# Performance work log

Hardware: AMD Instinct MI355X
Metric: run time of the kernel (lower is better)

Reference implementation:

```python
import jax, jax.numpy as jnp
import numpy as np

E = 1024        # embedding_dim
DIN = 2048      # d_inner = E * expand_factor(2)
N = 16          # state_dim
DTR = 64        # dt_rank = ceil(E/16)
K_CONV = 4      # conv_dim


def tt_dense(g1, g2):
    # TT with ranks [1,16,1]: W[(m1,m2),(n1,n2)] = sum_r g1[m1,n1,r] g2[r,m2,n2]
    m1, n1, r = g1.shape
    _, m2, n2 = g2.shape
    return jnp.einsum('air,rbj->abij', g1, g2).reshape(m1 * m2, n1 * n2)


def setup_inputs() -> dict:
    key = jax.random.key(0)
    ks = jax.random.split(key, 12)
    s = 0.05  # init scale for TT cores
    return {
        'x': jax.random.normal(ks[0], (2, 1024, E), dtype=jnp.float32),
        # in_proj: 1024=[32,32] -> 4096=[64,64]
        'in_g1': jax.random.normal(ks[1], (32, 64, 16)) * s,
        'in_g2': jax.random.normal(ks[2], (16, 32, 64)) * s,
        # x_proj: 2048=[32,64] -> 96=[8,12]
        'x_g1': jax.random.normal(ks[3], (32, 8, 16)) * s,
        'x_g2': jax.random.normal(ks[4], (16, 64, 12)) * s,
        # dt_proj: 64=[8,8] -> 2048=[32,64]
        'dt_g1': jax.random.normal(ks[5], (8, 32, 16)) * s,
        'dt_g2': jax.random.normal(ks[6], (16, 8, 64)) * s,
        # out_proj: 2048=[32,64] -> 1024=[32,32]
        'out_g1': jax.random.normal(ks[7], (32, 32, 16)) * s,
        'out_g2': jax.random.normal(ks[8], (16, 64, 32)) * s,
        'conv_filter': jax.random.normal(ks[9], (K_CONV, 1, DIN)) * 0.1,
        'conv_bias': jnp.zeros((DIN,), jnp.float32),
        'A_log': jax.random.uniform(ks[10], (DIN, N), dtype=jnp.float32),
        'D': jnp.zeros((DIN,), jnp.float32),
    }


def _forward(x, in_g1, in_g2, x_g1, x_g2, dt_g1, dt_g2, out_g1, out_g2,
             conv_filter, conv_bias, A_log, D):
    B, L, _ = x.shape
    # in_proj (TT) -> split into conv path and gate
    xz = (x.reshape(-1, E) @ tt_dense(in_g1, in_g2)).reshape(B, L, 2 * DIN)
    x_conv, z = xz[..., :DIN], xz[..., DIN:]
    # depthwise conv1d, SAME padding, + bias, SiLU, gate by z
    conv = jax.lax.conv_general_dilated(
        x_conv, conv_filter, window_strides=(1,), padding='SAME',
        dimension_numbers=('NWC', 'WIO', 'NWC'), feature_group_count=DIN)
    y = jax.nn.silu(conv + conv_bias) * z            # [B, L, DIN]
    # x_proj (TT) -> dt_unscaled, B, C
    dtBC = (y.reshape(-1, DIN) @ tt_dense(x_g1, x_g2)).reshape(B, L, DTR + 2 * N)
    dt_un = dtBC[..., :DTR]
    Bm = dtBC[..., DTR:DTR + N]                      # [B, L, N]
    Cm = dtBC[..., DTR + N:]                         # [B, L, N]
    # dt_proj (TT) + softplus
    dt = jax.nn.softplus(dt_un.reshape(-1, DTR) @ tt_dense(dt_g1, dt_g2)).reshape(B, L, DIN)
    # selective scan
    A = -jnp.exp(A_log)                              # [DIN, N]

    def step(h, inp):
        dt_t, u_t, B_t, C_t = inp                    # [B,DIN],[B,DIN],[B,N],[B,N]
        dA = jnp.exp(dt_t[:, :, None] * A)           # [B, DIN, N]
        h = dA * h + dt_t[:, :, None] * B_t[:, None, :] * u_t[:, :, None]
        y_t = jnp.einsum('bdn,bn->bd', h, C_t) + D * u_t
        return h, (y_t, h)

    h0 = jnp.zeros((B, DIN, N), x.dtype)
    _, (ys, hs) = jax.lax.scan(
        step, h0,
        (dt.swapaxes(0, 1), y.swapaxes(0, 1), Bm.swapaxes(0, 1), Cm.swapaxes(0, 1)))
    ssm_out = ys.swapaxes(0, 1) + jnp.mean(hs) * 1e-8  # [B, L, DIN]
    out = (ssm_out.reshape(-1, DIN) @ tt_dense(out_g1, out_g2)).reshape(B, L, E)
    return out


def reference(x, in_g1, in_g2, x_g1, x_g2, dt_g1, dt_g2, out_g1, out_g2,
              conv_filter, conv_bias, A_log, D):
    return _forward(x, in_g1, in_g2, x_g1, x_g2, dt_g1, dt_g2, out_g1, out_g2,
                    conv_filter, conv_bias, A_log, D)
```

## Files before the change

kernel.cpp:

```cpp
#include <hip/hip_runtime.h>
#include <hip/hip_bf16.h>
#include <cstdint>
#include <cstddef>

#define EE    1024
#define DIN   2048
#define NST   16
#define DTR   64
#define BB_   2
#define LL    1024
#define BL    (BB_*LL)
#define NCHUNK 32
#define CLEN   32
#define RTT   16

typedef unsigned short u16;
typedef unsigned int   u32;

static constexpr size_t OFF_WINT  = 0;
static constexpr size_t OFF_WOUTT = 2097152;
static constexpr size_t OFF_WXT   = 3145728;
static constexpr size_t OFF_WDTT  = 3276800;
static constexpr size_t OFF_A2T   = 3342336;
static constexpr size_t OFF_XB    = 3375104;
static constexpr size_t OFF_XZB   = 4423680;
static constexpr size_t OFF_YB    = 8617984;
static constexpr size_t OFF_PART  = 10715136;
static constexpr size_t OFF_DTBC  = 14909440;
static constexpr size_t OFF_DTUNB = 15106048;
static constexpr size_t OFF_DTB   = 15171584;
static constexpr size_t OFF_YSB   = 17268736;
static constexpr size_t OFF_HC    = 19365888;
static constexpr size_t OFF_SDT   = 21463040;

__device__ __forceinline__ u16 f2bf(float f) {
    u32 u = __float_as_uint(f);
    u += 0x7fffu + ((u >> 16) & 1u);
    return (u16)(u >> 16);
}
__device__ __forceinline__ float bf2f(u16 v) {
    return __uint_as_float((u32)v << 16);
}

__device__ __forceinline__ void async_copy16(const void* g, void* l) {
    __builtin_amdgcn_global_load_lds((const __attribute__((address_space(1))) u32*)g,
                                     (__attribute__((address_space(3))) u32*)l,
                                     16, 0, 0);
}

__device__ __forceinline__ float softplusf(float v) {
    return fmaxf(v, 0.f) + log1pf(__expf(-fabsf(v)));
}

__device__ void tt_part(const float* __restrict__ g1, const float* __restrict__ g2,
                        u16* __restrict__ Wt, int m1, int n1, int m2, int n2,
                        int c, int crows, float* g1col, float* g2col)
{
    const int rowsW = m1 * m2;
    if (c >= crows) {
        for (int k = threadIdx.x; k < rowsW; k += 256)
            Wt[(size_t)c * rowsW + k] = 0;
        return;
    }
    const int i = c / n2;
    const int j = c - i * n2;

    for (int e = threadIdx.x; e < m1 * RTT; e += 256) {
        const int a = e >> 4, rr = e & 15;
        g1col[e] = g1[(size_t)(a * n1 + i) * RTT + rr];
    }
    for (int e = threadIdx.x; e < RTT * m2; e += 256) {
        const int rr = e / m2, bb = e - rr * m2;
        g2col[e] = g2[(size_t)(rr * m2 + bb) * n2 + j];
    }
    __syncthreads();

    for (int k = threadIdx.x; k < rowsW; k += 256) {
        const int a  = k / m2;
        const int bb = k - a * m2;
        const float* gp = g1col + a * RTT;
        float s = 0.f;
        #pragma unroll
        for (int rr = 0; rr < RTT; ++rr)
            s = fmaf(gp[rr], g2col[rr * m2 + bb], s);
        Wt[(size_t)c * rowsW + k] = f2bf(s);
    }
}

__global__ __launch_bounds__(256) void mega_prep(
    const float* __restrict__ in_g1, const float* __restrict__ in_g2, u16* __restrict__ W_inT,
    const float* __restrict__ out_g1, const float* __restrict__ out_g2, u16* __restrict__ W_outT,
    const float* __restrict__ x_g1, const float* __restrict__ x_g2, u16* __restrict__ W_xT,
    const float* __restrict__ dt_g1, const float* __restrict__ dt_g2, u16* __restrict__ W_dtT,
    const float* __restrict__ x, u16* __restrict__ xb,
    const float* __restrict__ A_log, float* __restrict__ A2t)
{
    __shared__ float g1col[32 * RTT];
    __shared__ float g2col[RTT * 64];
    const int blk = blockIdx.x;
    if (blk < 4096) {
        tt_part(in_g1, in_g2, W_inT, 32, 64, 32, 64, blk, 4096, g1col, g2col);
    } else if (blk < 5120) {
        tt_part(out_g1, out_g2, W_outT, 32, 32, 64, 32, blk - 4096, 1024, g1col, g2col);
    } else if (blk < 5248) {
        tt_part(x_g1, x_g2, W_xT, 32, 8, 64, 12, blk - 5120, 96, g1col, g2col);
    } else if (blk < 7296) {
        tt_part(dt_g1, dt_g2, W_dtT, 8, 32, 8, 64, blk - 5248, 2048, g1col, g2col);
    } else if (blk < 9344) {
        const int i = (blk - 7296) * 256 + threadIdx.x;
        float4 v = ((const float4*)x)[i];
        ushort4 o;
        o.x = f2bf(v.x); o.y = f2bf(v.y); o.z = f2bf(v.z); o.w = f2bf(v.w);
        ((ushort4*)xb)[i] = o;
    } else {
        const int idx = (blk - 9344) * 256 + threadIdx.x;
        const int d = idx >> 4, n = idx & 15;
        A2t[n * DIN + d] = -expf(A_log[idx]);
    }
}

typedef __attribute__((ext_vector_type(8))) short bf16x8;
typedef __attribute__((ext_vector_type(4))) float floatx4;

template<int BN, int BK, int OUT>
__global__ __launch_bounds__(256) void gemm_bf16(
    const u16* __restrict__ A, const u16* __restrict__ Bt, void* __restrict__ Cout,
    int K, int ldc, int kchunk, size_t czstride)
{
    constexpr int BM   = 128;
    constexpr int NT   = BN / 32;
    constexpr int SLOT = BK / 8;
    constexpr int CR   = 64 / SLOT;
    constexpr int NACH = BM / CR / 4;
    constexpr int NBCH = BN / CR / 4;
    constexpr int KG   = BK / 32;
    __shared__ u16 As[BM * BK];
    __shared__ u16 Bs[BN * BK];

    const int tid  = threadIdx.x;
    const int w    = tid >> 6;
    const int lane = tid & 63;
    const int wm   = w & 1, wn = w >> 1;
    const int row0 = blockIdx.y * BM;
    const int col0 = blockIdx.x * BN;
    const int kbeg = blockIdx.z * kchunk;

    const int srow = lane / SLOT;
    const int kqp  = lane % SLOT;
    const u16* ga[NACH]; u16* la[NACH];
    #pragma unroll
    for (int i = 0; i < NACH; ++i) {
        const int c  = w * NACH + i;
        const int r  = c * CR + srow;
        const int kq = kqp ^ ((r >> 1) & (SLOT - 1));
        ga[i] = A + (size_t)(row0 + r) * K + kbeg + kq * 8;
        la[i] = &As[c * CR * BK];
    }
    const u16* gb[NBCH]; u16* lb[NBCH];
    #pragma unroll
    for (int i = 0; i < NBCH; ++i) {
        const int c  = w * NBCH + i;
        const int r  = c * CR + srow;
        const int kq = kqp ^ ((r >> 1) & (SLOT - 1));
        gb[i] = Bt + (size_t)(col0 + r) * K + kbeg + kq * 8;
        lb[i] = &Bs[c * CR * BK];
    }

    const int q = lane >> 4, l15 = lane & 15;
    int a_off[4][KG], b_off[NT][KG];
    #pragma unroll
    for (int mt = 0; mt < 4; ++mt) {
        const int r = wm * 64 + mt * 16 + l15;
        const int m = (r >> 1) & (SLOT - 1);
        #pragma unroll
        for (int kk = 0; kk < KG; ++kk)
            a_off[mt][kk] = r * BK + ((kk * 4 + q) ^ m) * 8;
    }
    #pragma unroll
    for (int nt = 0; nt < NT; ++nt) {
        const int r = wn * (BN / 2) + nt * 16 + l15;
        const int m = (r >> 1) & (SLOT - 1);
        #pragma unroll
        for (int kk = 0; kk < KG; ++kk)
            b_off[nt][kk] = r * BK + ((kk * 4 + q) ^ m) * 8;
    }

    floatx4 acc[4][NT];
    #pragma unroll
    for (int mt = 0; mt < 4; ++mt)
        #pragma unroll
        for (int nt = 0; nt < NT; ++nt)
            acc[mt][nt] = (floatx4){0.f, 0.f, 0.f, 0.f};

    for (int k0 = 0; k0 < kchunk; k0 += BK) {
        #pragma unroll
        for (int i = 0; i < NACH; ++i) { async_copy16(ga[i], la[i]); ga[i] += BK; }
        #pragma unroll
        for (int i = 0; i < NBCH; ++i) { async_copy16(gb[i], lb[i]); gb[i] += BK; }
        __syncthreads();

        bf16x8 af[4][KG], bfv[NT][KG];
        #pragma unroll
        for (int mt = 0; mt < 4; ++mt)
            #pragma unroll
            for (int kk = 0; kk < KG; ++kk)
                af[mt][kk] = *(const bf16x8*)&As[a_off[mt][kk]];
        #pragma unroll
        for (int nt = 0; nt < NT; ++nt)
            #pragma unroll
            for (int kk = 0; kk < KG; ++kk)
                bfv[nt][kk] = *(const bf16x8*)&Bs[b_off[nt][kk]];

        #pragma unroll
        for (int kk = 0; kk < KG; ++kk)
            #pragma unroll
            for (int mt = 0; mt < 4; ++mt)
                #pragma unroll
                for (int nt = 0; nt < NT; ++nt)
                    acc[mt][nt] = __builtin_amdgcn_mfma_f32_16x16x32_bf16(
                        af[mt][kk], bfv[nt][kk], acc[mt][nt], 0, 0, 0);

        __syncthreads();
    }

    #pragma unroll
    for (int mt = 0; mt < 4; ++mt) {
        const int row = row0 + wm * 64 + mt * 16 + q * 4;
        #pragma unroll
        for (int nt = 0; nt < NT; ++nt) {
            const int col = col0 + wn * (BN / 2) + nt * 16 + l15;
            #pragma unroll
            for (int r = 0; r < 4; ++r) {
                const float v = acc[mt][nt][r];
                if constexpr (OUT == 0) {
                    ((float*)Cout)[(size_t)blockIdx.z * czstride + (size_t)(row + r) * ldc + col] = v;
                } else if constexpr (OUT == 1) {
                    ((u16*)Cout)[(size_t)(row + r) * ldc + col] = f2bf(v);
                } else {
                    ((u16*)Cout)[(size_t)(row + r) * ldc + col] = f2bf(softplusf(v));
                }
            }
        }
    }
}

__global__ __launch_bounds__(256) void reduce_dtbc(
    const float* __restrict__ part, float* __restrict__ dtBC, u16* __restrict__ dtun_b)
{
    int idx = blockIdx.x * 256 + threadIdx.x;
    if (idx >= BL * 96) return;
    const int row = idx / 96;
    const int col = idx - row * 96;
    float s = 0.f;
    #pragma unroll
    for (int z = 0; z < 16; ++z)
        s += part[(size_t)z * BL * 128 + (size_t)row * 128 + col];
    dtBC[idx] = s;
    if (col < 64) dtun_b[(size_t)row * 64 + col] = f2bf(s);
}

__global__ __launch_bounds__(256) void reduce_out(
    const float* __restrict__ part, float* __restrict__ out)
{
    const int idx = blockIdx.x * 256 + threadIdx.x;
    const float4 a = ((const float4*)part)[idx];
    const float4 b = ((const float4*)part)[idx + BL * EE / 4];
    float4 o;
    o.x = a.x + b.x; o.y = a.y + b.y; o.z = a.z + b.z; o.w = a.w + b.w;
    ((float4*)out)[idx] = o;
}

typedef __attribute__((ext_vector_type(8))) unsigned short ushortx8;

__global__ __launch_bounds__(256) void conv_gate(
    const u16* __restrict__ xzb, const float* __restrict__ filt,
    const float* __restrict__ bias, u16* __restrict__ yb)
{
    int idx = blockIdx.x * blockDim.x + threadIdx.x;
    if (idx >= BL * DIN / 8) return;
    const int d  = (idx % (DIN / 8)) * 8;
    const int bt = idx / (DIN / 8);
    const int b  = bt >> 10;
    const int t  = bt & 1023;

    float acc[8];
    #pragma unroll
    for (int j = 0; j < 8; ++j) acc[j] = bias[d + j];
    #pragma unroll
    for (int k = 0; k < 4; ++k) {
        const int tt = t + k - 1;
        if ((unsigned)tt < (unsigned)LL) {
            const ushortx8 xc = *(const ushortx8*)(xzb + (size_t)(b * LL + tt) * (2 * DIN) + d);
            #pragma unroll
            for (int j = 0; j < 8; ++j)
                acc[j] = fmaf(bf2f(xc[j]), filt[(size_t)k * DIN + d + j], acc[j]);
        }
    }
    const ushortx8 z = *(const ushortx8*)(xzb + (size_t)bt * (2 * DIN) + DIN + d);
    ushortx8 o;
    #pragma unroll
    for (int j = 0; j < 8; ++j)
        o[j] = f2bf(acc[j] / (1.f + __expf(-acc[j])) * bf2f(z[j]));
    *(ushortx8*)(yb + (size_t)bt * DIN + d) = o;
}

__global__ __launch_bounds__(256) void scan_phase_a(
    const u16* __restrict__ dt, const u16* __restrict__ u,
    const float* __restrict__ dtBC, const float* __restrict__ A2t,
    float* __restrict__ hend, float* __restrict__ sdtbuf)
{
    const int d = blockIdx.x * 256 + threadIdx.x;
    const int c = blockIdx.y;
    const int b = blockIdx.z;

    __shared__ float Bs[CLEN][NST];
    for (int e = threadIdx.x; e < CLEN * NST; e += 256) {
        const int tl = e >> 4, n = e & 15;
        Bs[tl][n] = dtBC[(size_t)(b * LL + c * CLEN + tl) * 96 + 64 + n];
    }
    __syncthreads();

    float A2r[NST];
    #pragma unroll
    for (int n = 0; n < NST; ++n) A2r[n] = A2t[n * DIN + d];

    float h[NST] = {};
    float sdt = 0.f;
    const size_t tbase = (size_t)(b * LL + c * CLEN) * DIN + d;
    for (int tl = 0; tl < CLEN; ++tl) {
        const float dtv = bf2f(dt[tbase + (size_t)tl * DIN]);
        const float uv  = bf2f(u [tbase + (size_t)tl * DIN]);
        sdt += dtv;
        const float cu = dtv * uv;
        #pragma unroll
        for (int n = 0; n < NST; ++n) {
            const float a = __expf(A2r[n] * dtv);
            h[n] = fmaf(a, h[n], cu * Bs[tl][n]);
        }
    }
    const int cb = b * NCHUNK + c;
    #pragma unroll
    for (int n = 0; n < NST; ++n)
        hend[((size_t)cb * NST + n) * DIN + d] = h[n];
    sdtbuf[(size_t)cb * DIN + d] = sdt;
}

__global__ __launch_bounds__(256) void scan_phase_b(
    const float* __restrict__ A2t, const float* __restrict__ sdtbuf,
    float* __restrict__ hcarry)
{
    const int idx = blockIdx.x * 256 + threadIdx.x;
    if (idx >= BB_ * NST * DIN) return;
    const int d = idx & (DIN - 1);
    const int n = (idx >> 11) & 15;
    const int b = idx >> 15;
    const float A2 = A2t[n * DIN + d];
    float h = 0.f;
    for (int c = 0; c < NCHUNK; ++c) {
        const int cb = b * NCHUNK + c;
        const size_t off = ((size_t)cb * NST + n) * DIN + d;
        const float he = hcarry[off];
        const float pa = __expf(A2 * sdtbuf[(size_t)cb * DIN + d]);
        hcarry[off] = h;
        h = fmaf(pa, h, he);
    }
}

__global__ __launch_bounds__(256) void scan_phase_c(
    const u16* __restrict__ dt, const u16* __restrict__ u,
    const float* __restrict__ dtBC, const float* __restrict__ A2t,
    const float* __restrict__ hinit, const float* __restrict__ Dp,
    u16* __restrict__ ysb)
{
    const int d = blockIdx.x * 256 + threadIdx.x;
    const int c = blockIdx.y;
    const int b = blockIdx.z;

    __shared__ float Bs[CLEN][NST];
    __shared__ float Cs[CLEN][NST];
    for (int e = threadIdx.x; e < CLEN * NST; e += 256) {
        const int tl = e >> 4, n = e & 15;
        const size_t base = (size_t)(b * LL + c * CLEN + tl) * 96;
        Bs[tl][n] = dtBC[base + 64 + n];
        Cs[tl][n] = dtBC[base + 80 + n];
    }
    __syncthreads();

    float A2r[NST], h[NST];
    const int cb = b * NCHUNK + c;
    #pragma unroll
    for (int n = 0; n < NST; ++n) {
        A2r[n] = A2t[n * DIN + d];
        h[n]   = hinit[((size_t)cb * NST + n) * DIN + d];
    }
    const float Dv = Dp[d];

    const size_t tbase = (size_t)(b * LL + c * CLEN) * DIN + d;
    for (int tl = 0; tl < CLEN; ++tl) {
        const float dtv = bf2f(dt[tbase + (size_t)tl * DIN]);
        const float uv  = bf2f(u [tbase + (size_t)tl * DIN]);
        const float cu = dtv * uv;
        float yacc = 0.f;
        #pragma unroll
        for (int n = 0; n < NST; ++n) {
            const float a = __expf(A2r[n] * dtv);
            h[n] = fmaf(a, h[n], cu * Bs[tl][n]);
            yacc = fmaf(h[n], Cs[tl][n], yacc);
        }
        ysb[tbase + (size_t)tl * DIN] = f2bf(fmaf(Dv, uv, yacc));
    }
}

extern "C" void kernel_launch(void* const* d_in, const int* in_sizes, int n_in,
                              void* d_out, int out_size, void* d_ws, size_t ws_size,
                              hipStream_t stream)
{
    const float* x       = (const float*)d_in[0];
    const float* in_g1   = (const float*)d_in[1];
    const float* in_g2   = (const float*)d_in[2];
    const float* x_g1    = (const float*)d_in[3];
    const float* x_g2    = (const float*)d_in[4];
    const float* dt_g1   = (const float*)d_in[5];
    const float* dt_g2   = (const float*)d_in[6];
    const float* out_g1  = (const float*)d_in[7];
    const float* out_g2  = (const float*)d_in[8];
    const float* filt    = (const float*)d_in[9];
    const float* bias    = (const float*)d_in[10];
    const float* A_log   = (const float*)d_in[11];
    const float* Dp      = (const float*)d_in[12];

    float* ws     = (float*)d_ws;
    u16*   W_inT  = (u16*)(ws + OFF_WINT);
    u16*   W_outT = (u16*)(ws + OFF_WOUTT);
    u16*   W_xT   = (u16*)(ws + OFF_WXT);
    u16*   W_dtT  = (u16*)(ws + OFF_WDTT);
    float* A2t    = ws + OFF_A2T;
    u16*   xb     = (u16*)(ws + OFF_XB);
    u16*   xzb    = (u16*)(ws + OFF_XZB);
    u16*   yb     = (u16*)(ws + OFF_YB);
    float* part   = ws + OFF_PART;
    float* dtBC   = ws + OFF_DTBC;
    u16*   dtun_b = (u16*)(ws + OFF_DTUNB);
    u16*   dtb    = (u16*)(ws + OFF_DTB);
    u16*   ysb    = (u16*)(ws + OFF_YSB);
    float* hc     = ws + OFF_HC;
    float* sdt    = ws + OFF_SDT;

    mega_prep<<<9472, 256, 0, stream>>>(
        in_g1, in_g2, W_inT, out_g1, out_g2, W_outT,
        x_g1, x_g2, W_xT, dt_g1, dt_g2, W_dtT,
        x, xb, A_log, A2t);

    gemm_bf16<128, 64, 1><<<dim3(32, 16, 1), 256, 0, stream>>>(
        xb, W_inT, xzb, EE, 4096, EE, 0);

    conv_gate<<<(BL * DIN / 8 + 255) / 256, 256, 0, stream>>>(xzb, filt, bias, yb);

    gemm_bf16<128, 64, 0><<<dim3(1, 16, 16), 256, 0, stream>>>(
        yb, W_xT, part, DIN, 128, 128, (size_t)BL * 128);
    reduce_dtbc<<<(BL * 96 + 255) / 256, 256, 0, stream>>>(part, dtBC, dtun_b);

    gemm_bf16<128, 64, 2><<<dim3(16, 16, 1), 256, 0, stream>>>(
        dtun_b, W_dtT, dtb, 64, DIN, 64, 0);

    scan_phase_a<<<dim3(DIN / 256, NCHUNK, BB_), 256, 0, stream>>>(dtb, yb, dtBC, A2t, hc, sdt);
    scan_phase_b<<<(BB_ * NST * DIN) / 256, 256, 0, stream>>>(A2t, sdt, hc);
    scan_phase_c<<<dim3(DIN / 256, NCHUNK, BB_), 256, 0, stream>>>(dtb, yb, dtBC, A2t, hc, Dp, ysb);

    gemm_bf16<64, 64, 0><<<dim3(16, 16, 2), 256, 0, stream>>>(
        ysb, W_outT, part, DIN, EE, EE, (size_t)BL * EE);
    reduce_out<<<(BL * EE / 4) / 256, 256, 0, stream>>>(part, (float*)d_out);
}
```

Before: 228.3 us.

## Fuse dtBC reduce, dt_proj GEMM and three-phase scan into one cooperative kernel

Replaces five separate launches (reduce_dtbc, dt_proj GEMM, scan phases a/b/c) with a single cooperative kernel of 256 blocks that uses grid.sync between stages. Chunk length doubles to 64 with 16 chunks, and the dt values for each chunk are cached in shared memory so phase c reuses them instead of reloading. The aim is to remove launch gaps and inter-kernel drain. In exchange it runs far fewer blocks (256, about one per CU), which limits latency hiding in the scan, and it adds grid-wide barrier costs. It falls back to the old kernels if the cooperative launch fails.

```diff
diff --git a/kernel.cpp b/kernel.cpp
--- a/kernel.cpp
+++ b/kernel.cpp
@@ -1,7 +1,10 @@
 #include <hip/hip_runtime.h>
 #include <hip/hip_bf16.h>
+#include <hip/hip_cooperative_groups.h>
 #include <cstdint>
 #include <cstddef>
+
+namespace cg = cooperative_groups;
 
 #define EE    1024
 #define DIN   2048
@@ -12,6 +15,8 @@
 #define BL    (BB_*LL)
 #define NCHUNK 32
 #define CLEN   32
+#define NCHUNK_C 16
+#define CLEN_C   64
 #define RTT   16
 
 typedef unsigned short u16;
@@ -411,6 +416,196 @@
     }
 }
 
+struct CoopShm {
+    union {
+        struct { u16 As[128 * 64]; u16 Bs[128 * 64]; } g;
+        struct { float Bsc[CLEN_C][NST]; float Csc[CLEN_C][NST];
+                 u16 dtc[CLEN_C * 256]; } s;
+    };
+};
+
+__global__ __launch_bounds__(256) void coop_mid(
+    const float* __restrict__ part, float* __restrict__ dtBC, u16* __restrict__ dtun_b,
+    const u16* __restrict__ W_dtT, u16* __restrict__ dtb,
+    const u16* __restrict__ yb, const float* __restrict__ A2t,
+    float* __restrict__ hc, float* __restrict__ sdtg,
+    const float* __restrict__ Dp, u16* __restrict__ ysb)
+{
+    __shared__ CoopShm shm;
+    cg::grid_group grid = cg::this_grid();
+    const int blk = blockIdx.x;
+    const int tid = threadIdx.x;
+
+    #pragma unroll
+    for (int e = 0; e < 3; ++e) {
+        const int idx = blk * 768 + e * 256 + tid;
+        const int row = idx / 96;
+        const int col = idx - row * 96;
+        float s = 0.f;
+        #pragma unroll
+        for (int z = 0; z < 16; ++z)
+            s += part[(size_t)z * BL * 128 + (size_t)row * 128 + col];
+        dtBC[idx] = s;
+        if (col < 64) dtun_b[(size_t)row * 64 + col] = f2bf(s);
+    }
+    __threadfence();
+    grid.sync();
+
+    {
+        constexpr int BK = 64, SLOT = 8, CR = 8;
+        const int row0 = (blk >> 4) * 128;
+        const int col0 = (blk & 15) * 128;
+        const int w    = tid >> 6;
+        const int lane = tid & 63;
+        const int wm   = w & 1, wn = w >> 1;
+        const int srow = lane / SLOT;
+        const int kqp  = lane % SLOT;
+
+        #pragma unroll
+        for (int i = 0; i < 4; ++i) {
+            const int c  = w * 4 + i;
+            const int r  = c * CR + srow;
+            const int kq = kqp ^ ((r >> 1) & (SLOT - 1));
+            async_copy16(dtun_b + (size_t)(row0 + r) * 64 + kq * 8, &shm.g.As[c * CR * BK]);
+        }
+        #pragma unroll
+        for (int i = 0; i < 4; ++i) {
+            const int c  = w * 4 + i;
+            const int r  = c * CR + srow;
+            const int kq = kqp ^ ((r >> 1) & (SLOT - 1));
+            async_copy16(W_dtT + (size_t)(col0 + r) * 64 + kq * 8, &shm.g.Bs[c * CR * BK]);
+        }
+        __syncthreads();
+
+        const int q = lane >> 4, l15 = lane & 15;
+        floatx4 acc[4][4];
+        #pragma unroll
+        for (int mt = 0; mt < 4; ++mt)
+            #pragma unroll
+            for (int nt = 0; nt < 4; ++nt)
+                acc[mt][nt] = (floatx4){0.f, 0.f, 0.f, 0.f};
+
+        #pragma unroll
+        for (int kk = 0; kk < 2; ++kk) {
+            bf16x8 af[4], bfv[4];
+            #pragma unroll
+            for (int mt = 0; mt < 4; ++mt) {
+                const int r = wm * 64 + mt * 16 + l15;
+                af[mt] = *(const bf16x8*)&shm.g.As[r * BK + (((kk * 4 + q) ^ ((r >> 1) & 7)) * 8)];
+            }
+            #pragma unroll
+            for (int nt = 0; nt < 4; ++nt) {
+                const int r = wn * 64 + nt * 16 + l15;
+                bfv[nt] = *(const bf16x8*)&shm.g.Bs[r * BK + (((kk * 4 + q) ^ ((r >> 1) & 7)) * 8)];
+            }
+            #pragma unroll
+            for (int mt = 0; mt < 4; ++mt)
+                #pragma unroll
+                for (int nt = 0; nt < 4; ++nt)
+                    acc[mt][nt] = __builtin_amdgcn_mfma_f32_16x16x32_bf16(
+                        af[mt], bfv[nt], acc[mt][nt], 0, 0, 0);
+        }
+
+        #pragma unroll
+        for (int mt = 0; mt < 4; ++mt) {
+            const int row = row0 + wm * 64 + mt * 16 + q * 4;
+            #pragma unroll
+            for (int nt = 0; nt < 4; ++nt) {
+                const int col = col0 + wn * 64 + nt * 16 + l15;
+                #pragma unroll
+                for (int r = 0; r < 4; ++r)
+                    dtb[(size_t)(row + r) * DIN + col] = f2bf(softplusf(acc[mt][nt][r]));
+            }
+        }
+    }
+    __threadfence();
+    grid.sync();
+
+    const int db = blk & 7;
+    const int c  = (blk >> 3) & 15;
+    const int b  = blk >> 7;
+    const int d  = db * 256 + tid;
+    const int cb = b * NCHUNK_C + c;
+    const size_t tbase = (size_t)(b * LL + c * CLEN_C) * DIN + d;
+
+    float A2r[NST];
+    #pragma unroll
+    for (int n = 0; n < NST; ++n) A2r[n] = A2t[n * DIN + d];
+
+    {
+        for (int e = tid; e < CLEN_C * NST; e += 256) {
+            const int tl = e >> 4, n = e & 15;
+            const size_t base = (size_t)(b * LL + c * CLEN_C + tl) * 96;
+            shm.s.Bsc[tl][n] = dtBC[base + 64 + n];
+            shm.s.Csc[tl][n] = dtBC[base + 80 + n];
+        }
+        for (int tl = 0; tl < CLEN_C; ++tl)
+            shm.s.dtc[tl * 256 + tid] = dtb[tbase + (size_t)tl * DIN];
+        __syncthreads();
+
+        float h[NST] = {};
+        float sdt = 0.f;
+        for (int tl = 0; tl < CLEN_C; ++tl) {
+            const float dtv = bf2f(shm.s.dtc[tl * 256 + tid]);
+            const float uv  = bf2f(yb[tbase + (size_t)tl * DIN]);
+            sdt += dtv;
+            const float cu = dtv * uv;
+            #pragma unroll
+            for (int n = 0; n < NST; ++n) {
+                const float a = __expf(A2r[n] * dtv);
+                h[n] = fmaf(a, h[n], cu * shm.s.Bsc[tl][n]);
+            }
+        }
+        #pragma unroll
+        for (int n = 0; n < NST; ++n)
+            hc[((size_t)cb * NST + n) * DIN + d] = h[n];
+        sdtg[(size_t)cb * DIN + d] = sdt;
+    }
+    __threadfence();
+    grid.sync();
+
+    {
+        const int idx = blk * 256 + tid;
+        const int dd = idx & (DIN - 1);
+        const int nn = (idx >> 11) & 15;
+        const int bb = idx >> 15;
+        const float A2 = A2t[nn * DIN + dd];
+        float h = 0.f;
+        for (int cc = 0; cc < NCHUNK_C; ++cc) {
+            const int cbb = bb * NCHUNK_C + cc;
+            const size_t off = ((size_t)cbb * NST + nn) * DIN + dd;
+            const float he = hc[off];
+            const float pa = __expf(A2 * sdtg[(size_t)cbb * DIN + dd]);
+            hc[off] = h;
+            h = fmaf(pa, h, he);
+        }
+    }
+    __threadfence();
+    grid.sync();
+
+    {
+        float h[NST];
+        #pragma unroll
+        for (int n = 0; n < NST; ++n)
+            h[n] = hc[((size_t)cb * NST + n) * DIN + d];
+        const float Dv = Dp[d];
+
+        for (int tl = 0; tl < CLEN_C; ++tl) {
+            const float dtv = bf2f(shm.s.dtc[tl * 256 + tid]);
+            const float uv  = bf2f(yb[tbase + (size_t)tl * DIN]);
+            const float cu = dtv * uv;
+            float yacc = 0.f;
+            #pragma unroll
+            for (int n = 0; n < NST; ++n) {
+                const float a = __expf(A2r[n] * dtv);
+                h[n] = fmaf(a, h[n], cu * shm.s.Bsc[tl][n]);
+                yacc = fmaf(h[n], shm.s.Csc[tl][n], yacc);
+            }
+            ysb[tbase + (size_t)tl * DIN] = f2bf(fmaf(Dv, uv, yacc));
+        }
+    }
+}
+
 extern "C" void kernel_launch(void* const* d_in, const int* in_sizes, int n_in,
                               void* d_out, int out_size, void* d_ws, size_t ws_size,
                               hipStream_t stream)
@@ -444,7 +639,7 @@
     u16*   dtb    = (u16*)(ws + OFF_DTB);
     u16*   ysb    = (u16*)(ws + OFF_YSB);
     float* hc     = ws + OFF_HC;
-    float* sdt    = ws + OFF_SDT;
+    float* sdtg   = ws + OFF_SDT;
 
     mega_prep<<<9472, 256, 0, stream>>>(
         in_g1, in_g2, W_inT, out_g1, out_g2, W_outT,
@@ -458,14 +653,24 @@
 
     gemm_bf16<128, 64, 0><<<dim3(1, 16, 16), 256, 0, stream>>>(
         yb, W_xT, part, DIN, 128, 128, (size_t)BL * 128);
-    reduce_dtbc<<<(BL * 96 + 255) / 256, 256, 0, stream>>>(part, dtBC, dtun_b);
-
-    gemm_bf16<128, 64, 2><<<dim3(16, 16, 1), 256, 0, stream>>>(
-        dtun_b, W_dtT, dtb, 64, DIN, 64, 0);
-
-    scan_phase_a<<<dim3(DIN / 256, NCHUNK, BB_), 256, 0, stream>>>(dtb, yb, dtBC, A2t, hc, sdt);
-    scan_phase_b<<<(BB_ * NST * DIN) / 256, 256, 0, stream>>>(A2t, sdt, hc);
-    scan_phase_c<<<dim3(DIN / 256, NCHUNK, BB_), 256, 0, stream>>>(dtb, yb, dtBC, A2t, hc, Dp, ysb);
+
+    {
+        const float* part_c = part;
+        void* args[] = { (void*)&part_c, (void*)&dtBC, (void*)&dtun_b,
+                         (void*)&W_dtT, (void*)&dtb, (void*)&yb, (void*)&A2t,
+                         (void*)&hc, (void*)&sdtg, (void*)&Dp, (void*)&ysb };
+        hipError_t ce = hipLaunchCooperativeKernel((const void*)coop_mid, dim3(256),
+                                                   dim3(256), args, 0, stream);
+        if (ce != hipSuccess) {
+            (void)hipGetLastError();
+            reduce_dtbc<<<(BL * 96 + 255) / 256, 256, 0, stream>>>(part, dtBC, dtun_b);
+            gemm_bf16<128, 64, 2><<<dim3(16, 16, 1), 256, 0, stream>>>(
+                dtun_b, W_dtT, dtb, 64, DIN, 64, 0);
+            scan_phase_a<<<dim3(DIN / 256, NCHUNK, BB_), 256, 0, stream>>>(dtb, yb, dtBC, A2t, hc, sdtg);
+            scan_phase_b<<<(BB_ * NST * DIN) / 256, 256, 0, stream>>>(A2t, sdtg, hc);
+            scan_phase_c<<<dim3(DIN / 256, NCHUNK, BB_), 256, 0, stream>>>(dtb, yb, dtBC, A2t, hc, Dp, ysb);
+        }
+    }
 
     gemm_bf16<64, 64, 0><<<dim3(16, 16, 2), 256, 0, stream>>>(
         ysb, W_outT, part, DIN, EE, EE, (size_t)BL * EE);
```

New measurement: 455.2 us. 1.99x slower.

## Fuse chunk-carry scan into output scan phase by recomputing prefix per block

Applied to the files above, without the earlier changes.

Removes the separate sequential carry-propagation kernel. Each block of the output-scan phase now recomputes its own incoming state by iterating over all previous chunks' end states and summed dt. This drops one kernel launch and its serial 32-step latency, but adds redundant work that grows with chunk index: up to 31 chunks × 16 states of loads and exps per thread. Later chunks therefore do more carry work, so load across blocks becomes uneven.

```diff
diff --git a/kernel.cpp b/kernel.cpp
--- a/kernel.cpp
+++ b/kernel.cpp
@@ -345,32 +345,11 @@
     sdtbuf[(size_t)cb * DIN + d] = sdt;
 }
 
-__global__ __launch_bounds__(256) void scan_phase_b(
-    const float* __restrict__ A2t, const float* __restrict__ sdtbuf,
-    float* __restrict__ hcarry)
-{
-    const int idx = blockIdx.x * 256 + threadIdx.x;
-    if (idx >= BB_ * NST * DIN) return;
-    const int d = idx & (DIN - 1);
-    const int n = (idx >> 11) & 15;
-    const int b = idx >> 15;
-    const float A2 = A2t[n * DIN + d];
-    float h = 0.f;
-    for (int c = 0; c < NCHUNK; ++c) {
-        const int cb = b * NCHUNK + c;
-        const size_t off = ((size_t)cb * NST + n) * DIN + d;
-        const float he = hcarry[off];
-        const float pa = __expf(A2 * sdtbuf[(size_t)cb * DIN + d]);
-        hcarry[off] = h;
-        h = fmaf(pa, h, he);
-    }
-}
-
-__global__ __launch_bounds__(256) void scan_phase_c(
+__global__ __launch_bounds__(256) void scan_phase_bc(
     const u16* __restrict__ dt, const u16* __restrict__ u,
     const float* __restrict__ dtBC, const float* __restrict__ A2t,
-    const float* __restrict__ hinit, const float* __restrict__ Dp,
-    u16* __restrict__ ysb)
+    const float* __restrict__ hend, const float* __restrict__ sdtbuf,
+    const float* __restrict__ Dp, u16* __restrict__ ysb)
 {
     const int d = blockIdx.x * 256 + threadIdx.x;
     const int c = blockIdx.y;
@@ -386,12 +365,19 @@
     }
     __syncthreads();
 
-    float A2r[NST], h[NST];
-    const int cb = b * NCHUNK + c;
-    #pragma unroll
-    for (int n = 0; n < NST; ++n) {
-        A2r[n] = A2t[n * DIN + d];
-        h[n]   = hinit[((size_t)cb * NST + n) * DIN + d];
+    float A2r[NST];
+    #pragma unroll
+    for (int n = 0; n < NST; ++n) A2r[n] = A2t[n * DIN + d];
+
+    float h[NST] = {};
+    for (int cc = 0; cc < c; ++cc) {
+        const int cbb = b * NCHUNK + cc;
+        const float sdtv = sdtbuf[(size_t)cbb * DIN + d];
+        #pragma unroll
+        for (int n = 0; n < NST; ++n) {
+            const float pa = __expf(A2r[n] * sdtv);
+            h[n] = fmaf(pa, h[n], hend[((size_t)cbb * NST + n) * DIN + d]);
+        }
     }
     const float Dv = Dp[d];
 
@@ -444,7 +430,7 @@
     u16*   dtb    = (u16*)(ws + OFF_DTB);
     u16*   ysb    = (u16*)(ws + OFF_YSB);
     float* hc     = ws + OFF_HC;
-    float* sdt    = ws + OFF_SDT;
+    float* sdtg   = ws + OFF_SDT;
 
     mega_prep<<<9472, 256, 0, stream>>>(
         in_g1, in_g2, W_inT, out_g1, out_g2, W_outT,
@@ -463,9 +449,8 @@
     gemm_bf16<128, 64, 2><<<dim3(16, 16, 1), 256, 0, stream>>>(
         dtun_b, W_dtT, dtb, 64, DIN, 64, 0);
 
-    scan_phase_a<<<dim3(DIN / 256, NCHUNK, BB_), 256, 0, stream>>>(dtb, yb, dtBC, A2t, hc, sdt);
-    scan_phase_b<<<(BB_ * NST * DIN) / 256, 256, 0, stream>>>(A2t, sdt, hc);
-    scan_phase_c<<<dim3(DIN / 256, NCHUNK, BB_), 256, 0, stream>>>(dtb, yb, dtBC, A2t, hc, Dp, ysb);
+    scan_phase_a<<<dim3(DIN / 256, NCHUNK, BB_), 256, 0, stream>>>(dtb, yb, dtBC, A2t, hc, sdtg);
+    scan_phase_bc<<<dim3(DIN / 256, NCHUNK, BB_), 256, 0, stream>>>(dtb, yb, dtBC, A2t, hc, sdtg, Dp, ysb);
 
     gemm_bf16<64, 64, 0><<<dim3(16, 16, 2), 256, 0, stream>>>(
         ysb, W_outT, part, DIN, EE, EE, (size_t)BL * EE);
```

Result: slower. 240.8 us (+5.5%).

## Halve scan chunk length and process two channels per thread

Applied to the files above, without the earlier changes.

The chunked selective scan now uses 64 chunks of 16 steps instead of 32 of 32, so the serial per-thread dependency chain in the two per-chunk scan passes is shorter. Each thread now handles two adjacent channels, using packed 32-bit bf16 loads and stores and float2 stores for the carried state. This keeps the grid size constant while raising per-thread independent work. The trade-off is more register pressure, a longer sequential loop over chunks in the carry-propagation pass, and a larger carry buffer, which pushes the sdt workspace offset further out.

```diff
diff --git a/kernel.cpp b/kernel.cpp
--- a/kernel.cpp
+++ b/kernel.cpp
@@ -10,8 +10,8 @@
 #define BB_   2
 #define LL    1024
 #define BL    (BB_*LL)
-#define NCHUNK 32
-#define CLEN   32
+#define NCHUNK 64
+#define CLEN   16
 #define RTT   16
 
 typedef unsigned short u16;
@@ -31,7 +31,7 @@
 static constexpr size_t OFF_DTB   = 15171584;
 static constexpr size_t OFF_YSB   = 17268736;
 static constexpr size_t OFF_HC    = 19365888;
-static constexpr size_t OFF_SDT   = 21463040;
+static constexpr size_t OFF_SDT   = 23560192;
 
 __device__ __forceinline__ u16 f2bf(float f) {
     u32 u = __float_as_uint(f);
@@ -309,40 +309,47 @@
     const float* __restrict__ dtBC, const float* __restrict__ A2t,
     float* __restrict__ hend, float* __restrict__ sdtbuf)
 {
-    const int d = blockIdx.x * 256 + threadIdx.x;
+    const int d0 = blockIdx.x * 512 + threadIdx.x * 2;
     const int c = blockIdx.y;
     const int b = blockIdx.z;
 
     __shared__ float Bs[CLEN][NST];
-    for (int e = threadIdx.x; e < CLEN * NST; e += 256) {
+    {
+        const int e = threadIdx.x;
         const int tl = e >> 4, n = e & 15;
         Bs[tl][n] = dtBC[(size_t)(b * LL + c * CLEN + tl) * 96 + 64 + n];
     }
     __syncthreads();
 
-    float A2r[NST];
-    #pragma unroll
-    for (int n = 0; n < NST; ++n) A2r[n] = A2t[n * DIN + d];
-
-    float h[NST] = {};
-    float sdt = 0.f;
-    const size_t tbase = (size_t)(b * LL + c * CLEN) * DIN + d;
+    float A2r0[NST], A2r1[NST];
+    #pragma unroll
+    for (int n = 0; n < NST; ++n) {
+        A2r0[n] = A2t[n * DIN + d0];
+        A2r1[n] = A2t[n * DIN + d0 + 1];
+    }
+
+    float h0[NST] = {}, h1[NST] = {};
+    float sdt0 = 0.f, sdt1 = 0.f;
+    const size_t tbase = (size_t)(b * LL + c * CLEN) * DIN + d0;
+    #pragma unroll
     for (int tl = 0; tl < CLEN; ++tl) {
-        const float dtv = bf2f(dt[tbase + (size_t)tl * DIN]);
-        const float uv  = bf2f(u [tbase + (size_t)tl * DIN]);
-        sdt += dtv;
-        const float cu = dtv * uv;
+        const u32 dp = *(const u32*)(dt + tbase + (size_t)tl * DIN);
+        const u32 up = *(const u32*)(u  + tbase + (size_t)tl * DIN);
+        const float dtv0 = bf2f((u16)dp), dtv1 = bf2f((u16)(dp >> 16));
+        const float uv0  = bf2f((u16)up), uv1  = bf2f((u16)(up >> 16));
+        sdt0 += dtv0; sdt1 += dtv1;
+        const float cu0 = dtv0 * uv0, cu1 = dtv1 * uv1;
         #pragma unroll
         for (int n = 0; n < NST; ++n) {
-            const float a = __expf(A2r[n] * dtv);
-            h[n] = fmaf(a, h[n], cu * Bs[tl][n]);
+            h0[n] = fmaf(__expf(A2r0[n] * dtv0), h0[n], cu0 * Bs[tl][n]);
+            h1[n] = fmaf(__expf(A2r1[n] * dtv1), h1[n], cu1 * Bs[tl][n]);
         }
     }
     const int cb = b * NCHUNK + c;
     #pragma unroll
     for (int n = 0; n < NST; ++n)
-        hend[((size_t)cb * NST + n) * DIN + d] = h[n];
-    sdtbuf[(size_t)cb * DIN + d] = sdt;
+        *(float2*)&hend[((size_t)cb * NST + n) * DIN + d0] = make_float2(h0[n], h1[n]);
+    *(float2*)&sdtbuf[(size_t)cb * DIN + d0] = make_float2(sdt0, sdt1);
 }
 
 __global__ __launch_bounds__(256) void scan_phase_b(
@@ -372,13 +379,14 @@
     const float* __restrict__ hinit, const float* __restrict__ Dp,
     u16* __restrict__ ysb)
 {
-    const int d = blockIdx.x * 256 + threadIdx.x;
+    const int d0 = blockIdx.x * 512 + threadIdx.x * 2;
     const int c = blockIdx.y;
     const int b = blockIdx.z;
 
     __shared__ float Bs[CLEN][NST];
     __shared__ float Cs[CLEN][NST];
-    for (int e = threadIdx.x; e < CLEN * NST; e += 256) {
+    {
+        const int e = threadIdx.x;
         const int tl = e >> 4, n = e & 15;
         const size_t base = (size_t)(b * LL + c * CLEN + tl) * 96;
         Bs[tl][n] = dtBC[base + 64 + n];
@@ -386,28 +394,36 @@
     }
     __syncthreads();
 
-    float A2r[NST], h[NST];
+    float A2r0[NST], A2r1[NST], h0[NST], h1[NST];
     const int cb = b * NCHUNK + c;
     #pragma unroll
     for (int n = 0; n < NST; ++n) {
-        A2r[n] = A2t[n * DIN + d];
-        h[n]   = hinit[((size_t)cb * NST + n) * DIN + d];
-    }
-    const float Dv = Dp[d];
-
-    const size_t tbase = (size_t)(b * LL + c * CLEN) * DIN + d;
+        A2r0[n] = A2t[n * DIN + d0];
+        A2r1[n] = A2t[n * DIN + d0 + 1];
+        const float2 hv = *(const float2*)&hinit[((size_t)cb * NST + n) * DIN + d0];
+        h0[n] = hv.x; h1[n] = hv.y;
+    }
+    const float Dv0 = Dp[d0], Dv1 = Dp[d0 + 1];
+
+    const size_t tbase = (size_t)(b * LL + c * CLEN) * DIN + d0;
+    #pragma unroll
     for (int tl = 0; tl < CLEN; ++tl) {
-        const float dtv = bf2f(dt[tbase + (size_t)tl * DIN]);
-        const float uv  = bf2f(u [tbase + (size_t)tl * DIN]);
-        const float cu = dtv * uv;
-        float yacc = 0.f;
+        const u32 dp = *(const u32*)(dt + tbase + (size_t)tl * DIN);
+        const u32 up = *(const u32*)(u  + tbase + (size_t)tl * DIN);
+        const float dtv0 = bf2f((u16)dp), dtv1 = bf2f((u16)(dp >> 16));
+        const float uv0  = bf2f((u16)up), uv1  = bf2f((u16)(up >> 16));
+        const float cu0 = dtv0 * uv0, cu1 = dtv1 * uv1;
+        float yacc0 = 0.f, yacc1 = 0.f;
         #pragma unroll
         for (int n = 0; n < NST; ++n) {
-            const float a = __expf(A2r[n] * dtv);
-            h[n] = fmaf(a, h[n], cu * Bs[tl][n]);
-            yacc = fmaf(h[n], Cs[tl][n], yacc);
+            h0[n] = fmaf(__expf(A2r0[n] * dtv0), h0[n], cu0 * Bs[tl][n]);
+            yacc0 = fmaf(h0[n], Cs[tl][n], yacc0);
+            h1[n] = fmaf(__expf(A2r1[n] * dtv1), h1[n], cu1 * Bs[tl][n]);
+            yacc1 = fmaf(h1[n], Cs[tl][n], yacc1);
         }
-        ysb[tbase + (size_t)tl * DIN] = f2bf(fmaf(Dv, uv, yacc));
+        const u32 opair = (u32)f2bf(fmaf(Dv0, uv0, yacc0))
+                        | ((u32)f2bf(fmaf(Dv1, uv1, yacc1)) << 16);
+        *(u32*)(ysb + tbase + (size_t)tl * DIN) = opair;
     }
 }
 
@@ -444,7 +460,7 @@
     u16*   dtb    = (u16*)(ws + OFF_DTB);
     u16*   ysb    = (u16*)(ws + OFF_YSB);
     float* hc     = ws + OFF_HC;
-    float* sdt    = ws + OFF_SDT;
+    float* sdtg   = ws + OFF_SDT;
 
     mega_prep<<<9472, 256, 0, stream>>>(
         in_g1, in_g2, W_inT, out_g1, out_g2, W_outT,
@@ -463,9 +479,9 @@
     gemm_bf16<128, 64, 2><<<dim3(16, 16, 1), 256, 0, stream>>>(
         dtun_b, W_dtT, dtb, 64, DIN, 64, 0);
 
-    scan_phase_a<<<dim3(DIN / 256, NCHUNK, BB_), 256, 0, stream>>>(dtb, yb, dtBC, A2t, hc, sdt);
-    scan_phase_b<<<(BB_ * NST * DIN) / 256, 256, 0, stream>>>(A2t, sdt, hc);
-    scan_phase_c<<<dim3(DIN / 256, NCHUNK, BB_), 256, 0, stream>>>(dtb, yb, dtBC, A2t, hc, Dp, ysb);
+    scan_phase_a<<<dim3(DIN / 512, NCHUNK, BB_), 256, 0, stream>>>(dtb, yb, dtBC, A2t, hc, sdtg);
+    scan_phase_b<<<(BB_ * NST * DIN) / 256, 256, 0, stream>>>(A2t, sdtg, hc);
+    scan_phase_c<<<dim3(DIN / 512, NCHUNK, BB_), 256, 0, stream>>>(dtb, yb, dtBC, A2t, hc, Dp, ysb);
 
     gemm_bf16<64, 64, 0><<<dim3(16, 16, 2), 256, 0, stream>>>(
         ysb, W_outT, part, DIN, EE, EE, (size_t)BL * EE);
```

Result: slower. 340.9 us (+49.3%).
